# Kernel tuning notes

Measured on AMD Instinct MI355X. Metric: run time of the kernel, lower is better.

The kernel has to match this reference:

```python
import jax, jax.numpy as jnp
import numpy as np

N, T, IN, HID, ST, NL, OUT = 256, 2048, 6, 128, 64, 2, 6
LAY = IN + HID  # LMSCCell layer_size = input_size + hidden_size


def setup_inputs() -> dict:
    key = jax.random.key(0)
    ks = jax.random.split(key, 8)

    def w(k, shape, fan_in):
        return jax.random.normal(k, shape, jnp.float32) / np.sqrt(fan_in).astype(np.float32)

    return {
        "X": jax.random.normal(ks[0], (N, T, IN), jnp.float32),
        "H0": jax.random.normal(ks[1], (N, ST), jnp.float32),
        # NL gated layers (layer_size -> layer_size), stored stacked, weights as (in, out)
        "Wg1": w(ks[2], (NL, LAY, LAY), LAY), "bg1": jnp.zeros((NL, LAY), jnp.float32),
        "Wg2": w(ks[3], (NL, LAY, LAY), LAY), "bg2": jnp.zeros((NL, LAY), jnp.float32),
        # final pair: alpha (exp) and beta (tanh), layer_size -> hidden
        "Wa": w(ks[4], (LAY, HID), LAY), "ba": jnp.zeros((HID,), jnp.float32),
        "Wb": w(ks[5], (LAY, HID), LAY), "bb": jnp.zeros((HID,), jnp.float32),
        # hstate: Linear(state_size -> hidden) producing S0
        "Wh": w(ks[6], (ST, HID), ST), "bh": jnp.zeros((HID,), jnp.float32),
        # sstate2: Linear(hidden -> out_size)
        "Wo": w(ks[7], (HID, OUT), HID), "bo": jnp.zeros((OUT,), jnp.float32),
    }


def reference(X, H0, Wg1, bg1, Wg2, bg2, Wa, ba, Wb, bb, Wh, bh, Wo, bo):
    # hstate: initial hidden state for the LMSC recurrence
    S0 = H0 @ Wh + bh  # (N, HID)

    def step(H, x_t):
        # x_t: (N, IN); H: (N, HID)
        norm = jnp.linalg.norm(x_t, axis=1, keepdims=True)  # (N, 1)
        Lv = jnp.concatenate([x_t / norm, H], axis=1)       # (N, LAY)
        for i in range(NL):  # small fixed layer count, structurally distinct weights
            Lv = jnp.tanh(Lv @ Wg1[i] + bg1[i]) * jnp.tanh(Lv @ Wg2[i] + bg2[i])
        alpha = jnp.exp(Lv @ Wa + ba)   # (N, HID)
        beta = jnp.tanh(Lv @ Wb + bb)   # (N, HID)
        Hn = jnp.exp(-alpha * norm) * (H - beta) + beta
        return Hn, Hn

    _, Ys = jax.lax.scan(step, S0, jnp.swapaxes(X, 0, 1))  # (T, N, HID)
    Y = jnp.swapaxes(Ys, 0, 1)  # (N, T, HID)
    return Y @ Wo + bo          # (N, T, OUT)
```

## Files before the change

kernel.cpp:

```cpp
#include <hip/hip_runtime.h>

#define Nb   256
#define Tt   2048
#define INs  6
#define HID  128
#define STs  64
#define LAY  134
#define OUTs 6
#define NPAIR 67
#define NDW  68

typedef _Float16 h2 __attribute__((ext_vector_type(2)));
typedef __fp16  f16x2 __attribute__((ext_vector_type(2)));
typedef __fp16  f16x8 __attribute__((ext_vector_type(8)));

__device__ __forceinline__ float exp2_fast(float x) {
#if __has_builtin(__builtin_amdgcn_exp2f)
    return __builtin_amdgcn_exp2f(x);
#else
    return exp2f(x);
#endif
}
__device__ __forceinline__ float rcp_fast(float x) {
#if __has_builtin(__builtin_amdgcn_rcpf)
    return __builtin_amdgcn_rcpf(x);
#else
    return 1.0f / x;
#endif
}
__device__ __forceinline__ float tanh_fast(float x) {
    float e = exp2_fast(x * 2.8853900817779268f);
    return 1.0f - 2.0f * rcp_fast(e + 1.0f);
}
__device__ __forceinline__ unsigned pack2(float a, float b) {
#if __has_builtin(__builtin_amdgcn_cvt_pkrtz)
    union { f16x2 h; unsigned u; } u;
    u.h = __builtin_amdgcn_cvt_pkrtz(a, b);
    return u.u;
#else
    union { h2 h; unsigned u; } u;
    u.h[0] = (_Float16)a; u.h[1] = (_Float16)b;
    return u.u;
#endif
}
__device__ __forceinline__ float dot2p(unsigned av, f16x2 wv, float c) {
    union { unsigned u; f16x2 f; } ua; ua.u = av;
#if __has_builtin(__builtin_amdgcn_fdot2)
    return __builtin_amdgcn_fdot2(ua.f, wv, c, false);
#else
    return c + (float)ua.f[0] * (float)wv[0] + (float)ua.f[1] * (float)wv[1];
#endif
}

#define WR17(M) M(0) M(1) M(2) M(3) M(4) M(5) M(6) M(7) M(8) M(9) M(10) M(11) M(12) M(13) M(14) M(15) M(16)

#define DECLW(k) f16x8 w##k = {};

#define LOADW(k) { \
    f16x8 tmp; \
    _Pragma("unroll") \
    for (int q = 0; q < 8; ++q) { \
        int r = 8 * (k) + q; \
        float f = (r < LAY) ? Wp[r * od + j] : 0.f; \
        tmp[q] = (__fp16)f; \
    } \
    w##k = tmp; \
}

#define DOT4(k) { \
    uint4 v = b4[k]; \
    a0 = dot2p(v.x, __builtin_shufflevector(w##k, w##k, 0, 1), a0); \
    a1 = dot2p(v.y, __builtin_shufflevector(w##k, w##k, 2, 3), a1); \
    a2 = dot2p(v.z, __builtin_shufflevector(w##k, w##k, 4, 5), a2); \
    a3 = dot2p(v.w, __builtin_shufflevector(w##k, w##k, 6, 7), a3); \
}

#define DO_DOT(bufname, sres) { \
    const uint4* b4 = (const uint4*)(bufname); \
    float a0 = 0.f, a1 = 0.f, a2 = 0.f, a3 = 0.f; \
    WR17(DOT4) \
    sres = ((a0 + a1) + (a2 + a3)); \
}

__device__ __forceinline__ void do_proj(const float* Hrow, const float* Wol,
                                        const float* bol, float* outp, int l) {
    float hA = Hrow[2*l], hB = Hrow[2*l+1];
    float r[6];
#pragma unroll
    for (int o = 0; o < 6; ++o)
        r[o] = hA * Wol[(2*l) * OUTs + o] + hB * Wol[(2*l + 1) * OUTs + o];
#pragma unroll
    for (int o = 0; o < 6; ++o) {
#pragma unroll
        for (int k = 1; k < 64; k <<= 1) r[o] += __shfl_xor(r[o], k, 64);
    }
    if (l == 0) {
#pragma unroll
        for (int o = 0; o < 6; ++o) outp[o] = r[o] + bol[o];
    }
}

__global__ __launch_bounds__(1024) __attribute__((amdgpu_waves_per_eu(4, 4)))
void lmsc_kernel(const float* __restrict__ X,  const float* __restrict__ H0,
                 const float* __restrict__ Wg1, const float* __restrict__ bg1,
                 const float* __restrict__ Wg2, const float* __restrict__ bg2,
                 const float* __restrict__ Wa,  const float* __restrict__ ba,
                 const float* __restrict__ Wb,  const float* __restrict__ bb,
                 const float* __restrict__ Wh,  const float* __restrict__ bh,
                 const float* __restrict__ Wo,  const float* __restrict__ bo,
                 float* __restrict__ out)
{
    __shared__ float Xls[Tt * INs];
    __shared__ float ldspad[8192];
    __shared__ alignas(16) unsigned LvX[NDW];
    __shared__ alignas(16) unsigned LvB[NDW];
    __shared__ alignas(16) unsigned LvC[NDW];
    __shared__ float Hf[HID];
    __shared__ float H0l[STs];
    __shared__ float Wol[HID * OUTs];
    __shared__ float bol[OUTs];
    __shared__ float nrm[2], rnr[2];

    const int tid = threadIdx.x;
    const int n   = blockIdx.x;

    {
        unsigned lp = (unsigned)(unsigned long long)&ldspad[tid];
        asm volatile("" :: "v"(lp));
    }

    const bool isL1 = tid < 268;
    const bool isL2 = (tid >= 320) & (tid < 588);
    const bool isAB = (tid >= 640) & (tid < 896);
    const bool isPJ = (tid >= 896) & (tid < 960);

    {
        const float4* Xg  = (const float4*)(X + (size_t)n * (Tt * INs));
        float4*       Xl4 = (float4*)Xls;
        for (int i = tid; i < (Tt * INs) / 4; i += 1024) Xl4[i] = Xg[i];
    }
    if (tid < STs) H0l[tid] = H0[n * STs + tid];
    if (tid < HID * OUTs) Wol[tid] = Wo[tid];
    if (tid >= 1000 && tid < 1000 + OUTs) bol[tid - 1000] = bo[tid - 1000];
    if (tid == 1021) { LvX[NDW-1] = 0u; LvB[NDW-1] = 0u; LvC[NDW-1] = 0u; }

    WR17(DECLW)
    float bias = 0.f;
    {
        const float* Wp = nullptr; int od = LAY, j = 0;
        if (isL1) {
            j = tid >> 1;
            Wp = (tid & 1) ? Wg2 : Wg1;
            bias = ((tid & 1) ? bg2 : bg1)[j];
        } else if (isL2) {
            j = (tid - 320) >> 1;
            Wp = ((tid & 1) ? Wg2 : Wg1) + LAY * LAY;
            bias = ((tid & 1) ? bg2 : bg1)[LAY + j];
        } else if (isAB) {
            j = (tid - 640) >> 1;
            Wp = (tid & 1) ? Wb : Wa;  od = HID;
            bias = ((tid & 1) ? bb : ba)[j];
        }
        if (Wp) { WR17(LOADW) }
    }
    __syncthreads();

    float h = 0.f;
    if (isAB && !(tid & 1)) {
        int j = (tid - 640) >> 1;
        float s = bh[j];
        for (int k = 0; k < STs; ++k) s += H0l[k] * Wh[k * HID + j];
        h = s;
        Hf[j] = s;
        ((_Float16*)LvX)[6 + j] = (_Float16)s;
    }
    if (tid == 1022) {
        float s = 0.f;
#pragma unroll
        for (int i = 0; i < 6; ++i) s += Xls[i] * Xls[i];
        float nv = sqrtf(s);
        float rn = rcp_fast(nv);
        nrm[0] = nv; rnr[0] = rn;
        LvX[0] = pack2(Xls[0]*rn, Xls[1]*rn);
        LvX[1] = pack2(Xls[2]*rn, Xls[3]*rn);
        LvX[2] = pack2(Xls[4]*rn, Xls[5]*rn);
    }
    __syncthreads();

    const float LOG2E = 1.4426950408889634f;

#pragma unroll 1
    for (int t = 0; t < Tt; ++t) {
        const int p = t & 1;
        if (isL1) {
            float s; DO_DOT(LvX, s); s += bias;
            float tn = tanh_fast(s);
            float to = __shfl_xor(tn, 1, 64);
            if (!(tid & 1)) ((_Float16*)LvB)[tid >> 1] = (_Float16)(tn * to);
        } else if (isPJ) {
            if (t > 0)
                do_proj(Hf, Wol, bol, out + ((size_t)n * Tt + (t - 1)) * OUTs, tid - 896);
        } else if (tid == 1022 && (t + 1) < Tt) {
            const float* xp = &Xls[(t + 1) * INs];
            float s = 0.f;
#pragma unroll
            for (int i = 0; i < 6; ++i) s += xp[i] * xp[i];
            float nv = sqrtf(s);
            nrm[(t + 1) & 1] = nv;
            rnr[(t + 1) & 1] = rcp_fast(nv);
        }
        __syncthreads();
        if (isL2) {
            float s; DO_DOT(LvB, s); s += bias;
            float tn = tanh_fast(s);
            float to = __shfl_xor(tn, 1, 64);
            if (!(tid & 1)) ((_Float16*)LvC)[(tid - 320) >> 1] = (_Float16)(tn * to);
        } else if (tid == 1023 && (t + 1) < Tt) {
            const float* xp = &Xls[(t + 1) * INs];
            float rn = rnr[(t + 1) & 1];
            LvX[0] = pack2(xp[0]*rn, xp[1]*rn);
            LvX[1] = pack2(xp[2]*rn, xp[3]*rn);
            LvX[2] = pack2(xp[4]*rn, xp[5]*rn);
        }
        __syncthreads();
        if (isAB) {
            float s; DO_DOT(LvC, s); s += bias;
            float bown = tanh_fast(s);
            float beta = __shfl_xor(bown, 1, 64);
            if (!(tid & 1)) {
                int j = (tid - 640) >> 1;
                float alpha = exp2_fast(s * LOG2E);
                float e = exp2_fast(-alpha * nrm[p] * LOG2E);
                h = e * (h - beta) + beta;
                Hf[j] = h;
                ((_Float16*)LvX)[6 + j] = (_Float16)h;
            }
        }
        __syncthreads();
    }
    if (isPJ)
        do_proj(Hf, Wol, bol, out + ((size_t)n * Tt + (Tt - 1)) * OUTs, tid - 896);
}

extern "C" void kernel_launch(void* const* d_in, const int* in_sizes, int n_in,
                              void* d_out, int out_size, void* d_ws, size_t ws_size,
                              hipStream_t stream) {
    const float* X   = (const float*)d_in[0];
    const float* H0  = (const float*)d_in[1];
    const float* Wg1 = (const float*)d_in[2];
    const float* bg1 = (const float*)d_in[3];
    const float* Wg2 = (const float*)d_in[4];
    const float* bg2 = (const float*)d_in[5];
    const float* Wa  = (const float*)d_in[6];
    const float* ba  = (const float*)d_in[7];
    const float* Wb  = (const float*)d_in[8];
    const float* bb  = (const float*)d_in[9];
    const float* Wh  = (const float*)d_in[10];
    const float* bh  = (const float*)d_in[11];
    const float* Wo  = (const float*)d_in[12];
    const float* bo  = (const float*)d_in[13];
    float* out = (float*)d_out;

    hipLaunchKernelGGL(lmsc_kernel, dim3(Nb), dim3(1024), 0, stream,
                       X, H0, Wg1, bg1, Wg2, bg2, Wa, ba, Wb, bb, Wh, bh, Wo, bo, out);
}
```

Before: 3.575 ms.

## Shrink block to 512 threads with split alpha/beta dots and LDS-streamed overflow rows

Recasts the per-sequence recurrence from 1024 threads to 512. Each thread now holds one 128-column gated-layer weight slice plus half of an alpha/beta column, so the alpha/beta dot is split across thread pairs. The 12 leftover gate columns (128..133) are computed by spare threads that stream packed weights from LDS. This adds one barrier per step, because beta goes through shared memory before the state update. The aim is to allow two blocks per CU instead of one and to drop the LDS padding array, at the cost of more register pressure and extra synchronisation in the serial step.

```diff
diff --git a/kernel.cpp b/kernel.cpp
--- a/kernel.cpp
+++ b/kernel.cpp
@@ -7,12 +7,11 @@
 #define STs  64
 #define LAY  134
 #define OUTs 6
-#define NPAIR 67
 #define NDW  68
 
-typedef _Float16 h2 __attribute__((ext_vector_type(2)));
-typedef __fp16  f16x2 __attribute__((ext_vector_type(2)));
-typedef __fp16  f16x8 __attribute__((ext_vector_type(8)));
+typedef __fp16 f16x2 __attribute__((ext_vector_type(2)));
+typedef __fp16 f16x4 __attribute__((ext_vector_type(4)));
+typedef __fp16 f16x8 __attribute__((ext_vector_type(8)));
 
 __device__ __forceinline__ float exp2_fast(float x) {
 #if __has_builtin(__builtin_amdgcn_exp2f)
@@ -38,10 +37,15 @@
     u.h = __builtin_amdgcn_cvt_pkrtz(a, b);
     return u.u;
 #else
-    union { h2 h; unsigned u; } u;
-    u.h[0] = (_Float16)a; u.h[1] = (_Float16)b;
+    union { f16x2 h; unsigned u; } u;
+    u.h[0] = (__fp16)a; u.h[1] = (__fp16)b;
     return u.u;
 #endif
+}
+__device__ __forceinline__ unsigned pack2w(float a, float b) {
+    union { f16x2 h; unsigned u; } u;
+    u.h[0] = (__fp16)a; u.h[1] = (__fp16)b;
+    return u.u;
 }
 __device__ __forceinline__ float dot2p(unsigned av, f16x2 wv, float c) {
     union { unsigned u; f16x2 f; } ua; ua.u = av;
@@ -51,56 +55,65 @@
     return c + (float)ua.f[0] * (float)wv[0] + (float)ua.f[1] * (float)wv[1];
 #endif
 }
+__device__ __forceinline__ float dotdw(unsigned av, unsigned wv, float c) {
+    union { unsigned u; f16x2 f; } uw; uw.u = wv;
+    return dot2p(av, uw.f, c);
+}
+
+__device__ __forceinline__ float stream_dot(const unsigned* act, const unsigned* wcol) {
+    const uint4* a4 = (const uint4*)act;
+    const uint4* w4 = (const uint4*)wcol;
+    float a0 = 0.f, a1 = 0.f, a2 = 0.f, a3 = 0.f;
+#pragma unroll
+    for (int k = 0; k < 17; ++k) {
+        uint4 av = a4[k], wv = w4[k];
+        a0 = dotdw(av.x, wv.x, a0);
+        a1 = dotdw(av.y, wv.y, a1);
+        a2 = dotdw(av.z, wv.z, a2);
+        a3 = dotdw(av.w, wv.w, a3);
+    }
+    return (a0 + a1) + (a2 + a3);
+}
 
 #define WR17(M) M(0) M(1) M(2) M(3) M(4) M(5) M(6) M(7) M(8) M(9) M(10) M(11) M(12) M(13) M(14) M(15) M(16)
 
 #define DECLW(k) f16x8 w##k = {};
+#define DECLP(k) f16x4 p##k = {};
 
 #define LOADW(k) { \
     f16x8 tmp; \
     _Pragma("unroll") \
     for (int q = 0; q < 8; ++q) { \
         int r = 8 * (k) + q; \
-        float f = (r < LAY) ? Wp[r * od + j] : 0.f; \
+        float f = (r < LAY) ? Wp[r * LAY + j] : 0.f; \
         tmp[q] = (__fp16)f; \
     } \
     w##k = tmp; \
 }
-
-#define DOT4(k) { \
+#define LOADP(k) { \
+    f16x4 tmp; \
+    _Pragma("unroll") \
+    for (int q = 0; q < 4; ++q) { \
+        int r = hb + 4 * (k) + q; \
+        float f = (r < LAY) ? Wp3[r * HID + u] : 0.f; \
+        tmp[q] = (__fp16)f; \
+    } \
+    p##k = tmp; \
+}
+#define DOTW(k) { \
     uint4 v = b4[k]; \
     a0 = dot2p(v.x, __builtin_shufflevector(w##k, w##k, 0, 1), a0); \
     a1 = dot2p(v.y, __builtin_shufflevector(w##k, w##k, 2, 3), a1); \
     a2 = dot2p(v.z, __builtin_shufflevector(w##k, w##k, 4, 5), a2); \
     a3 = dot2p(v.w, __builtin_shufflevector(w##k, w##k, 6, 7), a3); \
 }
-
-#define DO_DOT(bufname, sres) { \
-    const uint4* b4 = (const uint4*)(bufname); \
-    float a0 = 0.f, a1 = 0.f, a2 = 0.f, a3 = 0.f; \
-    WR17(DOT4) \
-    sres = ((a0 + a1) + (a2 + a3)); \
-}
-
-__device__ __forceinline__ void do_proj(const float* Hrow, const float* Wol,
-                                        const float* bol, float* outp, int l) {
-    float hA = Hrow[2*l], hB = Hrow[2*l+1];
-    float r[6];
-#pragma unroll
-    for (int o = 0; o < 6; ++o)
-        r[o] = hA * Wol[(2*l) * OUTs + o] + hB * Wol[(2*l + 1) * OUTs + o];
-#pragma unroll
-    for (int o = 0; o < 6; ++o) {
-#pragma unroll
-        for (int k = 1; k < 64; k <<= 1) r[o] += __shfl_xor(r[o], k, 64);
-    }
-    if (l == 0) {
-#pragma unroll
-        for (int o = 0; o < 6; ++o) outp[o] = r[o] + bol[o];
-    }
-}
-
-__global__ __launch_bounds__(1024) __attribute__((amdgpu_waves_per_eu(4, 4)))
+#define DOTP(k) { \
+    uint2 v = c2[k]; \
+    q0 = dot2p(v.x, __builtin_shufflevector(p##k, p##k, 0, 1), q0); \
+    q1 = dot2p(v.y, __builtin_shufflevector(p##k, p##k, 2, 3), q1); \
+}
+
+__global__ __launch_bounds__(512, 2)
 void lmsc_kernel(const float* __restrict__ X,  const float* __restrict__ H0,
                  const float* __restrict__ Wg1, const float* __restrict__ bg1,
                  const float* __restrict__ Wg2, const float* __restrict__ bg2,
@@ -111,76 +124,87 @@
                  float* __restrict__ out)
 {
     __shared__ float Xls[Tt * INs];
-    __shared__ float ldspad[8192];
+    __shared__ unsigned OvW1[12][NDW];
+    __shared__ unsigned OvW2[12][NDW];
     __shared__ alignas(16) unsigned LvX[NDW];
     __shared__ alignas(16) unsigned LvB[NDW];
     __shared__ alignas(16) unsigned LvC[NDW];
     __shared__ float Hf[HID];
+    __shared__ float Bbe[HID];
     __shared__ float H0l[STs];
-    __shared__ float Wol[HID * OUTs];
+    __shared__ float WolT[OUTs][HID];
     __shared__ float bol[OUTs];
     __shared__ float nrm[2], rnr[2];
 
     const int tid = threadIdx.x;
     const int n   = blockIdx.x;
 
-    {
-        unsigned lp = (unsigned)(unsigned long long)&ldspad[tid];
-        asm volatile("" :: "v"(lp));
-    }
-
-    const bool isL1 = tid < 268;
-    const bool isL2 = (tid >= 320) & (tid < 588);
-    const bool isAB = (tid >= 640) & (tid < 896);
-    const bool isPJ = (tid >= 896) & (tid < 960);
+    const bool G1  = tid < 256;
+    const int  u   = (tid & 255) >> 1;
+    const int  odd = tid & 1;
 
     {
         const float4* Xg  = (const float4*)(X + (size_t)n * (Tt * INs));
         float4*       Xl4 = (float4*)Xls;
-        for (int i = tid; i < (Tt * INs) / 4; i += 1024) Xl4[i] = Xg[i];
+        for (int i = tid; i < (Tt * INs) / 4; i += 512) Xl4[i] = Xg[i];
     }
     if (tid < STs) H0l[tid] = H0[n * STs + tid];
-    if (tid < HID * OUTs) Wol[tid] = Wo[tid];
-    if (tid >= 1000 && tid < 1000 + OUTs) bol[tid - 1000] = bo[tid - 1000];
-    if (tid == 1021) { LvX[NDW-1] = 0u; LvB[NDW-1] = 0u; LvC[NDW-1] = 0u; }
+    for (int i = tid; i < OUTs * HID; i += 512) {
+        int o = i / HID, l2 = i % HID;
+        WolT[o][l2] = Wo[l2 * OUTs + o];
+    }
+    if (tid < OUTs) bol[tid] = bo[tid];
+    if (tid == 30) { LvX[NDW-1] = 0u; LvB[NDW-1] = 0u; LvC[NDW-1] = 0u; }
+    if (tid >= 32 && tid < 56) {
+        int i  = tid - 32;
+        int L  = i / 12, s9 = i % 12, pp = s9 >> 1, mt = s9 & 1;
+        const float* src = (mt ? Wg2 : Wg1) + L * LAY * LAY;
+        unsigned* dst = L ? OvW2[s9] : OvW1[s9];
+        for (int d = 0; d < 67; ++d)
+            dst[d] = pack2w(src[(2*d) * LAY + 128 + pp], src[(2*d+1) * LAY + 128 + pp]);
+        dst[67] = 0u;
+    }
 
     WR17(DECLW)
-    float bias = 0.f;
+    WR17(DECLP)
+    float breg, pb;
     {
-        const float* Wp = nullptr; int od = LAY, j = 0;
-        if (isL1) {
-            j = tid >> 1;
-            Wp = (tid & 1) ? Wg2 : Wg1;
-            bias = ((tid & 1) ? bg2 : bg1)[j];
-        } else if (isL2) {
-            j = (tid - 320) >> 1;
-            Wp = ((tid & 1) ? Wg2 : Wg1) + LAY * LAY;
-            bias = ((tid & 1) ? bg2 : bg1)[LAY + j];
-        } else if (isAB) {
-            j = (tid - 640) >> 1;
-            Wp = (tid & 1) ? Wb : Wa;  od = HID;
-            bias = ((tid & 1) ? bb : ba)[j];
-        }
-        if (Wp) { WR17(LOADW) }
+        const float* Wp = (odd ? Wg2 : Wg1) + (G1 ? 0 : LAY * LAY);
+        const int j = u;
+        WR17(LOADW)
+        breg = (odd ? bg2 : bg1)[(G1 ? 0 : LAY) + j];
+        const float* Wp3 = G1 ? Wa : Wb;
+        const int hb = odd ? 68 : 0;
+        WR17(LOADP)
+        pb = (G1 ? ba : bb)[u];
+    }
+    float sb = 0.f;
+    if (tid >= 256 && tid < 268) {
+        int s9 = tid - 256;
+        sb = ((s9 & 1) ? bg2 : bg1)[128 + (s9 >> 1)];
+    } else if (tid < 12) {
+        sb = (odd ? bg2 : bg1)[LAY + 128 + (tid >> 1)];
     }
     __syncthreads();
 
-    float h = 0.f;
-    if (isAB && !(tid & 1)) {
-        int j = (tid - 640) >> 1;
-        float s = bh[j];
-        for (int k = 0; k < STs; ++k) s += H0l[k] * Wh[k * HID + j];
+    float h = 0.f, s3 = 0.f;
+    if (G1 && !odd) {
+        float s = bh[u];
+        for (int k = 0; k < STs; ++k) s += H0l[k] * Wh[k * HID + u];
         h = s;
-        Hf[j] = s;
-        ((_Float16*)LvX)[6 + j] = (_Float16)s;
-    }
-    if (tid == 1022) {
+        Hf[u] = s;
+        ((__fp16*)LvX)[6 + u] = (__fp16)s;
+    }
+    if (tid == 500) {
         float s = 0.f;
 #pragma unroll
         for (int i = 0; i < 6; ++i) s += Xls[i] * Xls[i];
         float nv = sqrtf(s);
-        float rn = rcp_fast(nv);
-        nrm[0] = nv; rnr[0] = rn;
+        nrm[0] = nv; rnr[0] = rcp_fast(nv);
+    }
+    __syncthreads();
+    if (tid == 1) {
+        float rn = rnr[0];
         LvX[0] = pack2(Xls[0]*rn, Xls[1]*rn);
         LvX[1] = pack2(Xls[2]*rn, Xls[3]*rn);
         LvX[2] = pack2(Xls[4]*rn, Xls[5]*rn);
@@ -191,16 +215,43 @@
 
 #pragma unroll 1
     for (int t = 0; t < Tt; ++t) {
-        const int p = t & 1;
-        if (isL1) {
-            float s; DO_DOT(LvX, s); s += bias;
+        if (G1) {
+            const uint4* b4 = (const uint4*)LvX;
+            float a0 = 0.f, a1 = 0.f, a2 = 0.f, a3 = 0.f;
+            WR17(DOTW)
+            float s  = ((a0 + a1) + (a2 + a3)) + breg;
             float tn = tanh_fast(s);
             float to = __shfl_xor(tn, 1, 64);
-            if (!(tid & 1)) ((_Float16*)LvB)[tid >> 1] = (_Float16)(tn * to);
-        } else if (isPJ) {
-            if (t > 0)
-                do_proj(Hf, Wol, bol, out + ((size_t)n * Tt + (t - 1)) * OUTs, tid - 896);
-        } else if (tid == 1022 && (t + 1) < Tt) {
+            if (!odd) ((__fp16*)LvB)[u] = (__fp16)(tn * to);
+        } else if (tid < 268) {
+            int s9 = tid - 256;
+            float sd = stream_dot(LvX, OvW1[s9]) + sb;
+            float tn = tanh_fast(sd);
+            float to = __shfl_xor(tn, 1, 64);
+            if (!odd) ((__fp16*)LvB)[128 + (s9 >> 1)] = (__fp16)(tn * to);
+        } else if (tid >= 320 && tid < 384) {
+            if (t > 0) {
+                int l = tid - 320;
+                float hA = Hf[2*l], hB = Hf[2*l+1];
+                float r0 = hA*WolT[0][2*l] + hB*WolT[0][2*l+1];
+                float r1 = hA*WolT[1][2*l] + hB*WolT[1][2*l+1];
+                float r2 = hA*WolT[2][2*l] + hB*WolT[2][2*l+1];
+                float r3 = hA*WolT[3][2*l] + hB*WolT[3][2*l+1];
+                float r4 = hA*WolT[4][2*l] + hB*WolT[4][2*l+1];
+                float r5 = hA*WolT[5][2*l] + hB*WolT[5][2*l+1];
+#pragma unroll
+                for (int k = 1; k < 64; k <<= 1) {
+                    r0 += __shfl_xor(r0, k, 64); r1 += __shfl_xor(r1, k, 64);
+                    r2 += __shfl_xor(r2, k, 64); r3 += __shfl_xor(r3, k, 64);
+                    r4 += __shfl_xor(r4, k, 64); r5 += __shfl_xor(r5, k, 64);
+                }
+                if (l == 0) {
+                    float* op = out + ((size_t)n * Tt + (t - 1)) * OUTs;
+                    op[0] = r0 + bol[0]; op[1] = r1 + bol[1]; op[2] = r2 + bol[2];
+                    op[3] = r3 + bol[3]; op[4] = r4 + bol[4]; op[5] = r5 + bol[5];
+                }
+            }
+        } else if (tid == 500 && (t + 1) < Tt) {
             const float* xp = &Xls[(t + 1) * INs];
             float s = 0.f;
 #pragma unroll
@@ -210,12 +261,41 @@
             rnr[(t + 1) & 1] = rcp_fast(nv);
         }
         __syncthreads();
-        if (isL2) {
-            float s; DO_DOT(LvB, s); s += bias;
+        if (!G1) {
+            const uint4* b4 = (const uint4*)LvB;
+            float a0 = 0.f, a1 = 0.f, a2 = 0.f, a3 = 0.f;
+            WR17(DOTW)
+            float s  = ((a0 + a1) + (a2 + a3)) + breg;
             float tn = tanh_fast(s);
             float to = __shfl_xor(tn, 1, 64);
-            if (!(tid & 1)) ((_Float16*)LvC)[(tid - 320) >> 1] = (_Float16)(tn * to);
-        } else if (tid == 1023 && (t + 1) < Tt) {
+            if (!odd) ((__fp16*)LvC)[u] = (__fp16)(tn * to);
+        } else if (tid < 12) {
+            float sd = stream_dot(LvB, OvW2[tid]) + sb;
+            float tn = tanh_fast(sd);
+            float to = __shfl_xor(tn, 1, 64);
+            if (!odd) ((__fp16*)LvC)[128 + (tid >> 1)] = (__fp16)(tn * to);
+        }
+        __syncthreads();
+        {
+            const uint2* c2 = (const uint2*)LvC + (odd ? 17 : 0);
+            float q0 = 0.f, q1 = 0.f;
+            WR17(DOTP)
+            float pd = q0 + q1;
+            pd += __shfl_xor(pd, 1, 64);
+            if (!odd) {
+                s3 = pd + pb;
+                if (!G1) Bbe[u] = tanh_fast(s3);
+            }
+        }
+        __syncthreads();
+        if (G1 && !odd) {
+            float alpha = exp2_fast(s3 * LOG2E);
+            float beta  = Bbe[u];
+            float e = exp2_fast(-alpha * nrm[t & 1] * LOG2E);
+            h = e * (h - beta) + beta;
+            Hf[u] = h;
+            ((__fp16*)LvX)[6 + u] = (__fp16)h;
+        } else if (tid == 1 && (t + 1) < Tt) {
             const float* xp = &Xls[(t + 1) * INs];
             float rn = rnr[(t + 1) & 1];
             LvX[0] = pack2(xp[0]*rn, xp[1]*rn);
@@ -223,23 +303,28 @@
             LvX[2] = pack2(xp[4]*rn, xp[5]*rn);
         }
         __syncthreads();
-        if (isAB) {
-            float s; DO_DOT(LvC, s); s += bias;
-            float bown = tanh_fast(s);
-            float beta = __shfl_xor(bown, 1, 64);
-            if (!(tid & 1)) {
-                int j = (tid - 640) >> 1;
-                float alpha = exp2_fast(s * LOG2E);
-                float e = exp2_fast(-alpha * nrm[p] * LOG2E);
-                h = e * (h - beta) + beta;
-                Hf[j] = h;
-                ((_Float16*)LvX)[6 + j] = (_Float16)h;
-            }
-        }
-        __syncthreads();
-    }
-    if (isPJ)
-        do_proj(Hf, Wol, bol, out + ((size_t)n * Tt + (Tt - 1)) * OUTs, tid - 896);
+    }
+    if (tid >= 320 && tid < 384) {
+        int l = tid - 320;
+        float hA = Hf[2*l], hB = Hf[2*l+1];
+        float r0 = hA*WolT[0][2*l] + hB*WolT[0][2*l+1];
+        float r1 = hA*WolT[1][2*l] + hB*WolT[1][2*l+1];
+        float r2 = hA*WolT[2][2*l] + hB*WolT[2][2*l+1];
+        float r3 = hA*WolT[3][2*l] + hB*WolT[3][2*l+1];
+        float r4 = hA*WolT[4][2*l] + hB*WolT[4][2*l+1];
+        float r5 = hA*WolT[5][2*l] + hB*WolT[5][2*l+1];
+#pragma unroll
+        for (int k = 1; k < 64; k <<= 1) {
+            r0 += __shfl_xor(r0, k, 64); r1 += __shfl_xor(r1, k, 64);
+            r2 += __shfl_xor(r2, k, 64); r3 += __shfl_xor(r3, k, 64);
+            r4 += __shfl_xor(r4, k, 64); r5 += __shfl_xor(r5, k, 64);
+        }
+        if (l == 0) {
+            float* op = out + ((size_t)n * Tt + (Tt - 1)) * OUTs;
+            op[0] = r0 + bol[0]; op[1] = r1 + bol[1]; op[2] = r2 + bol[2];
+            op[3] = r3 + bol[3]; op[4] = r4 + bol[4]; op[5] = r5 + bol[5];
+        }
+    }
 }
 
 extern "C" void kernel_launch(void* const* d_in, const int* in_sizes, int n_in,
@@ -261,6 +346,6 @@
     const float* bo  = (const float*)d_in[13];
     float* out = (float*)d_out;
 
-    hipLaunchKernelGGL(lmsc_kernel, dim3(Nb), dim3(1024), 0, stream,
+    hipLaunchKernelGGL(lmsc_kernel, dim3(Nb), dim3(512), 0, stream,
                        X, H0, Wg1, bg1, Wg2, bg2, Wa, ba, Wb, bb, Wh, bh, Wo, bo, out);
 }
```

Result: faster. 3.402 ms (-4.8%).

## Split each dot product across thread pairs with all weights in registers

Applied to the files above, without the earlier changes.

The block is cut from 1024 to 512 threads. Every thread now keeps weight slices for all three stages (both gated layers and the alpha/beta layer) in registers, and each output column's dot product is split across two threads combined with a shuffle. The leftover 6 columns of the 134-wide layers go to a few threads reading packed weights from LDS. The output projection is batched: 32 timesteps of hidden state are buffered in LDS and flushed together, replacing the per-step projection wave. This shortens the serial chain of each stage and removes idle role-specialised waves, at the cost of higher register pressure and an extra shuffle per stage.

```diff
diff --git a/kernel.cpp b/kernel.cpp
--- a/kernel.cpp
+++ b/kernel.cpp
@@ -7,12 +7,11 @@
 #define STs  64
 #define LAY  134
 #define OUTs 6
-#define NPAIR 67
-#define NDW  68
-
-typedef _Float16 h2 __attribute__((ext_vector_type(2)));
-typedef __fp16  f16x2 __attribute__((ext_vector_type(2)));
-typedef __fp16  f16x8 __attribute__((ext_vector_type(8)));
+#define VDW  72
+#define HB_ODD 72
+
+typedef __fp16 f16x2 __attribute__((ext_vector_type(2)));
+typedef __fp16 f16x8 __attribute__((ext_vector_type(8)));
 
 __device__ __forceinline__ float exp2_fast(float x) {
 #if __has_builtin(__builtin_amdgcn_exp2f)
@@ -38,10 +37,15 @@
     u.h = __builtin_amdgcn_cvt_pkrtz(a, b);
     return u.u;
 #else
-    union { h2 h; unsigned u; } u;
-    u.h[0] = (_Float16)a; u.h[1] = (_Float16)b;
+    union { f16x2 h; unsigned u; } u;
+    u.h[0] = (__fp16)a; u.h[1] = (__fp16)b;
     return u.u;
 #endif
+}
+__device__ __forceinline__ unsigned pack2w(float a, float b) {
+    union { f16x2 h; unsigned u; } u;
+    u.h[0] = (__fp16)a; u.h[1] = (__fp16)b;
+    return u.u;
 }
 __device__ __forceinline__ float dot2p(unsigned av, f16x2 wv, float c) {
     union { unsigned u; f16x2 f; } ua; ua.u = av;
@@ -51,56 +55,36 @@
     return c + (float)ua.f[0] * (float)wv[0] + (float)ua.f[1] * (float)wv[1];
 #endif
 }
-
-#define WR17(M) M(0) M(1) M(2) M(3) M(4) M(5) M(6) M(7) M(8) M(9) M(10) M(11) M(12) M(13) M(14) M(15) M(16)
-
-#define DECLW(k) f16x8 w##k = {};
-
-#define LOADW(k) { \
-    f16x8 tmp; \
-    _Pragma("unroll") \
-    for (int q = 0; q < 8; ++q) { \
-        int r = 8 * (k) + q; \
-        float f = (r < LAY) ? Wp[r * od + j] : 0.f; \
-        tmp[q] = (__fp16)f; \
-    } \
-    w##k = tmp; \
-}
-
-#define DOT4(k) { \
-    uint4 v = b4[k]; \
-    a0 = dot2p(v.x, __builtin_shufflevector(w##k, w##k, 0, 1), a0); \
-    a1 = dot2p(v.y, __builtin_shufflevector(w##k, w##k, 2, 3), a1); \
-    a2 = dot2p(v.z, __builtin_shufflevector(w##k, w##k, 4, 5), a2); \
-    a3 = dot2p(v.w, __builtin_shufflevector(w##k, w##k, 6, 7), a3); \
-}
-
-#define DO_DOT(bufname, sres) { \
-    const uint4* b4 = (const uint4*)(bufname); \
-    float a0 = 0.f, a1 = 0.f, a2 = 0.f, a3 = 0.f; \
-    WR17(DOT4) \
-    sres = ((a0 + a1) + (a2 + a3)); \
-}
-
-__device__ __forceinline__ void do_proj(const float* Hrow, const float* Wol,
-                                        const float* bol, float* outp, int l) {
-    float hA = Hrow[2*l], hB = Hrow[2*l+1];
-    float r[6];
-#pragma unroll
-    for (int o = 0; o < 6; ++o)
-        r[o] = hA * Wol[(2*l) * OUTs + o] + hB * Wol[(2*l + 1) * OUTs + o];
-#pragma unroll
-    for (int o = 0; o < 6; ++o) {
-#pragma unroll
-        for (int k = 1; k < 64; k <<= 1) r[o] += __shfl_xor(r[o], k, 64);
-    }
-    if (l == 0) {
-#pragma unroll
-        for (int o = 0; o < 6; ++o) outp[o] = r[o] + bol[o];
-    }
-}
-
-__global__ __launch_bounds__(1024) __attribute__((amdgpu_waves_per_eu(4, 4)))
+__device__ __forceinline__ float dotdw(unsigned av, unsigned wv, float c) {
+    union { unsigned u; f16x2 f; } uw; uw.u = wv;
+    return dot2p(av, uw.f, c);
+}
+
+#define DECLW(P) f16x8 P##0={},P##1={},P##2={},P##3={},P##4={},P##5={},P##6={},P##7={},P##8={}
+
+#define LOADW1(P,k,Wsrc,od,colv,hbv) { f16x8 tmp; \
+    _Pragma("unroll") for (int q=0;q<8;++q){ int r=(hbv)+8*(k)+q; \
+        float f=(r<LAY)?(Wsrc)[r*(od)+(colv)]:0.f; tmp[q]=(__fp16)f; } P##k=tmp; }
+#define LOADSET(P,Wsrc,od,colv,hbv) \
+    LOADW1(P,0,Wsrc,od,colv,hbv) LOADW1(P,1,Wsrc,od,colv,hbv) LOADW1(P,2,Wsrc,od,colv,hbv) \
+    LOADW1(P,3,Wsrc,od,colv,hbv) LOADW1(P,4,Wsrc,od,colv,hbv) LOADW1(P,5,Wsrc,od,colv,hbv) \
+    LOADW1(P,6,Wsrc,od,colv,hbv) LOADW1(P,7,Wsrc,od,colv,hbv) LOADW1(P,8,Wsrc,od,colv,hbv)
+
+#define DOTK(P,k) { \
+    a0=dot2p(x##k.x,__builtin_shufflevector(P##k,P##k,0,1),a0); \
+    a1=dot2p(x##k.y,__builtin_shufflevector(P##k,P##k,2,3),a1); \
+    a2=dot2p(x##k.z,__builtin_shufflevector(P##k,P##k,4,5),a2); \
+    a3=dot2p(x##k.w,__builtin_shufflevector(P##k,P##k,6,7),a3); }
+#define DOTSET(P) DOTK(P,0) DOTK(P,1) DOTK(P,2) DOTK(P,3) DOTK(P,4) DOTK(P,5) DOTK(P,6) DOTK(P,7) DOTK(P,8)
+
+#define LOADX(buf) const uint4* a4_=(const uint4*)(buf)+hoff9; \
+    uint4 x0=a4_[0],x1=a4_[1],x2=a4_[2],x3=a4_[3],x4=a4_[4],x5=a4_[5],x6=a4_[6],x7=a4_[7],x8=a4_[8]
+
+#define OVK(k) { uint4 wv=w4_[k]; o0=dotdw(x##k.x,wv.x,o0); o1=dotdw(x##k.y,wv.y,o1); \
+                 o2=dotdw(x##k.z,wv.z,o2); o3=dotdw(x##k.w,wv.w,o3); }
+#define OVSET OVK(0) OVK(1) OVK(2) OVK(3) OVK(4) OVK(5) OVK(6) OVK(7) OVK(8)
+
+__global__ __launch_bounds__(512, 1) __attribute__((amdgpu_waves_per_eu(2, 2)))
 void lmsc_kernel(const float* __restrict__ X,  const float* __restrict__ H0,
                  const float* __restrict__ Wg1, const float* __restrict__ bg1,
                  const float* __restrict__ Wg2, const float* __restrict__ bg2,
@@ -111,76 +95,83 @@
                  float* __restrict__ out)
 {
     __shared__ float Xls[Tt * INs];
-    __shared__ float ldspad[8192];
-    __shared__ alignas(16) unsigned LvX[NDW];
-    __shared__ alignas(16) unsigned LvB[NDW];
-    __shared__ alignas(16) unsigned LvC[NDW];
-    __shared__ float Hf[HID];
+    __shared__ alignas(16) float Hhist[32][HID];
+    __shared__ alignas(16) float WolT[OUTs][HID];
     __shared__ float H0l[STs];
-    __shared__ float Wol[HID * OUTs];
     __shared__ float bol[OUTs];
-    __shared__ float nrm[2], rnr[2];
-
-    const int tid = threadIdx.x;
-    const int n   = blockIdx.x;
-
-    {
-        unsigned lp = (unsigned)(unsigned long long)&ldspad[tid];
-        asm volatile("" :: "v"(lp));
-    }
-
-    const bool isL1 = tid < 268;
-    const bool isL2 = (tid >= 320) & (tid < 588);
-    const bool isAB = (tid >= 640) & (tid < 896);
-    const bool isPJ = (tid >= 896) & (tid < 960);
+    __shared__ alignas(16) unsigned OvW1[12][VDW];
+    __shared__ alignas(16) unsigned OvW2[12][VDW];
+    __shared__ alignas(16) unsigned LvX[VDW];
+    __shared__ alignas(16) unsigned LvB[VDW];
+    __shared__ alignas(16) unsigned LvC[VDW];
+    __shared__ float nrm[2];
+
+    const int tid  = threadIdx.x;
+    const int n    = blockIdx.x;
+    const int half = tid & 1;
+    const int mat  = (tid >> 1) & 1;
+    const int col  = tid >> 2;
+    const int hoff9 = half * 9;
+    const int hb    = half * HB_ODD;
+    __fp16* LvX16 = (__fp16*)LvX;
+    __fp16* LvB16 = (__fp16*)LvB;
+    __fp16* LvC16 = (__fp16*)LvC;
 
     {
         const float4* Xg  = (const float4*)(X + (size_t)n * (Tt * INs));
         float4*       Xl4 = (float4*)Xls;
-        for (int i = tid; i < (Tt * INs) / 4; i += 1024) Xl4[i] = Xg[i];
+        for (int i = tid; i < (Tt * INs) / 4; i += 512) Xl4[i] = Xg[i];
     }
     if (tid < STs) H0l[tid] = H0[n * STs + tid];
-    if (tid < HID * OUTs) Wol[tid] = Wo[tid];
-    if (tid >= 1000 && tid < 1000 + OUTs) bol[tid - 1000] = bo[tid - 1000];
-    if (tid == 1021) { LvX[NDW-1] = 0u; LvB[NDW-1] = 0u; LvC[NDW-1] = 0u; }
-
-    WR17(DECLW)
-    float bias = 0.f;
-    {
-        const float* Wp = nullptr; int od = LAY, j = 0;
-        if (isL1) {
-            j = tid >> 1;
-            Wp = (tid & 1) ? Wg2 : Wg1;
-            bias = ((tid & 1) ? bg2 : bg1)[j];
-        } else if (isL2) {
-            j = (tid - 320) >> 1;
-            Wp = ((tid & 1) ? Wg2 : Wg1) + LAY * LAY;
-            bias = ((tid & 1) ? bg2 : bg1)[LAY + j];
-        } else if (isAB) {
-            j = (tid - 640) >> 1;
-            Wp = (tid & 1) ? Wb : Wa;  od = HID;
-            bias = ((tid & 1) ? bb : ba)[j];
-        }
-        if (Wp) { WR17(LOADW) }
-    }
+    for (int i = tid; i < OUTs * HID; i += 512) {
+        int o = i >> 7, l2 = i & 127;
+        WolT[o][l2] = Wo[l2 * OUTs + o];
+    }
+    if (tid < OUTs) bol[tid] = bo[tid];
+    if (tid < 5) LvX[67 + tid] = 0u;
+    else if (tid < 10) LvB[62 + tid] = 0u;
+    else if (tid < 15) LvC[57 + tid] = 0u;
+    if (tid >= 64 && tid < 88) {
+        int i = tid - 64; int L = (i >= 12); int d = i - L * 12;
+        int c = 128 + (d >> 1); int m = d & 1;
+        const float* src = (m ? Wg2 : Wg1) + L * LAY * LAY;
+        unsigned* dst = L ? OvW2[d] : OvW1[d];
+        for (int q = 0; q < VDW; ++q) {
+            int r0 = 2 * q, r1 = 2 * q + 1;
+            float f0 = (r0 < LAY) ? src[r0 * LAY + c] : 0.f;
+            float f1 = (r1 < LAY) ? src[r1 * LAY + c] : 0.f;
+            dst[q] = pack2w(f0, f1);
+        }
+    }
+
+    DECLW(u); DECLW(v); DECLW(p);
+    const float* Wgm = mat ? Wg2 : Wg1;
+    LOADSET(u, Wgm, LAY, col, hb);
+    LOADSET(v, Wgm + LAY * LAY, LAY, col, hb);
+    const float* Wab = mat ? Wb : Wa;
+    LOADSET(p, Wab, HID, col, hb);
+    float gb0 = (mat ? bg2 : bg1)[col];
+    float gb1 = (mat ? bg2 : bg1)[LAY + col];
+    float pb  = (mat ? bb : ba)[col];
+    float ovb = 0.f;
+    if (tid < 24)        ovb = (((tid >> 1) & 1) ? bg2 : bg1)[128 + (tid >> 2)];
+    else if (tid >= 488) { int e = tid - 488; ovb = (((e >> 1) & 1) ? bg2 : bg1)[LAY + 128 + (e >> 2)]; }
+
     __syncthreads();
 
     float h = 0.f;
-    if (isAB && !(tid & 1)) {
-        int j = (tid - 640) >> 1;
-        float s = bh[j];
-        for (int k = 0; k < STs; ++k) s += H0l[k] * Wh[k * HID + j];
+    if ((tid & 3) == 0) {
+        float s = bh[col];
+        for (int k = 0; k < STs; ++k) s += H0l[k] * Wh[k * HID + col];
         h = s;
-        Hf[j] = s;
-        ((_Float16*)LvX)[6 + j] = (_Float16)s;
-    }
-    if (tid == 1022) {
+        LvX16[6 + col] = (__fp16)s;
+    }
+    if (tid == 56) {
         float s = 0.f;
 #pragma unroll
         for (int i = 0; i < 6; ++i) s += Xls[i] * Xls[i];
-        float nv = sqrtf(s);
-        float rn = rcp_fast(nv);
-        nrm[0] = nv; rnr[0] = rn;
+        float nv = sqrtf(s), rn = rcp_fast(nv);
+        nrm[0] = nv;
         LvX[0] = pack2(Xls[0]*rn, Xls[1]*rn);
         LvX[1] = pack2(Xls[2]*rn, Xls[3]*rn);
         LvX[2] = pack2(Xls[4]*rn, Xls[5]*rn);
@@ -191,55 +182,100 @@
 
 #pragma unroll 1
     for (int t = 0; t < Tt; ++t) {
-        const int p = t & 1;
-        if (isL1) {
-            float s; DO_DOT(LvX, s); s += bias;
+        unsigned nx0 = 0, nx1 = 0, nx2 = 0;
+        {
+            LOADX(LvX);
+            float a0 = 0.f, a1 = 0.f, a2 = 0.f, a3 = 0.f;
+            DOTSET(u);
+            float s = (a0 + a1) + (a2 + a3);
+            s += __shfl_xor(s, 1, 64);
+            s += gb0;
             float tn = tanh_fast(s);
-            float to = __shfl_xor(tn, 1, 64);
-            if (!(tid & 1)) ((_Float16*)LvB)[tid >> 1] = (_Float16)(tn * to);
-        } else if (isPJ) {
-            if (t > 0)
-                do_proj(Hf, Wol, bol, out + ((size_t)n * Tt + (t - 1)) * OUTs, tid - 896);
-        } else if (tid == 1022 && (t + 1) < Tt) {
-            const float* xp = &Xls[(t + 1) * INs];
-            float s = 0.f;
+            float to = __shfl_xor(tn, 2, 64);
+            if ((tid & 3) == 0) LvB16[col] = (__fp16)(tn * to);
+            if (tid < 24) {
+                const uint4* w4_ = (const uint4*)OvW1[tid >> 1] + hoff9;
+                float o0 = 0.f, o1 = 0.f, o2 = 0.f, o3 = 0.f;
+                OVSET;
+                float so = (o0 + o1) + (o2 + o3);
+                so += __shfl_xor(so, 1, 64);
+                so += ovb;
+                float tno = tanh_fast(so);
+                float too = __shfl_xor(tno, 2, 64);
+                if ((tid & 3) == 0) LvB16[128 + (tid >> 2)] = (__fp16)(tno * too);
+            } else if (tid == 56 && (t + 1) < Tt) {
+                const float* xp = &Xls[(t + 1) * INs];
+                float s2 = 0.f;
 #pragma unroll
-            for (int i = 0; i < 6; ++i) s += xp[i] * xp[i];
-            float nv = sqrtf(s);
-            nrm[(t + 1) & 1] = nv;
-            rnr[(t + 1) & 1] = rcp_fast(nv);
+                for (int i = 0; i < 6; ++i) s2 += xp[i] * xp[i];
+                float nv = sqrtf(s2), rn = rcp_fast(nv);
+                nrm[(t + 1) & 1] = nv;
+                nx0 = pack2(xp[0]*rn, xp[1]*rn);
+                nx1 = pack2(xp[2]*rn, xp[3]*rn);
+                nx2 = pack2(xp[4]*rn, xp[5]*rn);
+            }
         }
         __syncthreads();
-        if (isL2) {
-            float s; DO_DOT(LvB, s); s += bias;
+        {
+            LOADX(LvB);
+            float a0 = 0.f, a1 = 0.f, a2 = 0.f, a3 = 0.f;
+            DOTSET(v);
+            float s = (a0 + a1) + (a2 + a3);
+            s += __shfl_xor(s, 1, 64);
+            s += gb1;
             float tn = tanh_fast(s);
-            float to = __shfl_xor(tn, 1, 64);
-            if (!(tid & 1)) ((_Float16*)LvC)[(tid - 320) >> 1] = (_Float16)(tn * to);
-        } else if (tid == 1023 && (t + 1) < Tt) {
-            const float* xp = &Xls[(t + 1) * INs];
-            float rn = rnr[(t + 1) & 1];
-            LvX[0] = pack2(xp[0]*rn, xp[1]*rn);
-            LvX[1] = pack2(xp[2]*rn, xp[3]*rn);
-            LvX[2] = pack2(xp[4]*rn, xp[5]*rn);
+            float to = __shfl_xor(tn, 2, 64);
+            if ((tid & 3) == 0) LvC16[col] = (__fp16)(tn * to);
+            if (tid >= 488) {
+                int e = tid - 488;
+                const uint4* w4_ = (const uint4*)OvW2[e >> 1] + hoff9;
+                float o0 = 0.f, o1 = 0.f, o2 = 0.f, o3 = 0.f;
+                OVSET;
+                float so = (o0 + o1) + (o2 + o3);
+                so += __shfl_xor(so, 1, 64);
+                so += ovb;
+                float tno = tanh_fast(so);
+                float too = __shfl_xor(tno, 2, 64);
+                if ((e & 3) == 0) LvC16[128 + (e >> 2)] = (__fp16)(tno * too);
+            } else if (tid == 56 && (t + 1) < Tt) {
+                LvX[0] = nx0; LvX[1] = nx1; LvX[2] = nx2;
+            }
         }
         __syncthreads();
-        if (isAB) {
-            float s; DO_DOT(LvC, s); s += bias;
-            float bown = tanh_fast(s);
-            float beta = __shfl_xor(bown, 1, 64);
-            if (!(tid & 1)) {
-                int j = (tid - 640) >> 1;
+        {
+            LOADX(LvC);
+            float a0 = 0.f, a1 = 0.f, a2 = 0.f, a3 = 0.f;
+            DOTSET(p);
+            float s = (a0 + a1) + (a2 + a3);
+            s += __shfl_xor(s, 1, 64);
+            s += pb;
+            float tn = tanh_fast(s);
+            float beta = __shfl_xor(tn, 2, 64);
+            if ((tid & 3) == 0) {
                 float alpha = exp2_fast(s * LOG2E);
-                float e = exp2_fast(-alpha * nrm[p] * LOG2E);
-                h = e * (h - beta) + beta;
-                Hf[j] = h;
-                ((_Float16*)LvX)[6 + j] = (_Float16)h;
+                float e2 = exp2_fast(-alpha * nrm[t & 1] * LOG2E);
+                h = e2 * (h - beta) + beta;
+                Hhist[t & 31][col] = h;
+                LvX16[6 + col] = (__fp16)h;
             }
         }
         __syncthreads();
-    }
-    if (isPJ)
-        do_proj(Hf, Wol, bol, out + ((size_t)n * Tt + (Tt - 1)) * OUTs, tid - 896);
+        if ((t & 31) == 31) {
+            if (tid < 192) {
+                int fs = tid / 6, fo = tid - fs * 6;
+                float acc = bol[fo];
+                const float4* hr = (const float4*)(&Hhist[fs][0]);
+                const float4* wr = (const float4*)(&WolT[fo][0]);
+#pragma unroll
+                for (int k2 = 0; k2 < HID / 4; ++k2) {
+                    float4 hv = hr[k2], wv = wr[k2];
+                    acc += hv.x*wv.x + hv.y*wv.y + hv.z*wv.z + hv.w*wv.w;
+                }
+                out[((size_t)n * Tt + (t - 31) + fs) * OUTs + fo] = acc;
+            }
+            __syncthreads();
+        }
+    }
 }
 
 extern "C" void kernel_launch(void* const* d_in, const int* in_sizes, int n_in,
@@ -261,6 +297,6 @@
     const float* bo  = (const float*)d_in[13];
     float* out = (float*)d_out;
 
-    hipLaunchKernelGGL(lmsc_kernel, dim3(Nb), dim3(1024), 0, stream,
+    hipLaunchKernelGGL(lmsc_kernel, dim3(Nb), dim3(512), 0, stream,
                        X, H0, Wg1, bg1, Wg2, bg2, Wa, ba, Wb, bb, Wh, bh, Wo, bo, out);
 }
```

Measured after the change: 3.987 ms. 1.12x slower.
